# Performance work log

Measured on AMD Instinct MI355X. Metric: run time of the kernel, lower is better.

Reference implementation:

```python
import jax, jax.numpy as jnp
import numpy as np

B, C, H = 65536, 512, 8
HD = C // H  # head dim = 64
SCALE = HD ** -0.5


def setup_inputs() -> dict:
    key = jax.random.key(0)
    k1, k2, k3, k4 = jax.random.split(key, 4)
    x = jax.random.normal(k1, (B, 2, C), dtype=jnp.float32)
    W_kv = jax.random.normal(k2, (C, 2 * C), dtype=jnp.float32) * (C ** -0.5)
    W_proj = jax.random.normal(k3, (C, C), dtype=jnp.float32) * (C ** -0.5)
    b_proj = jax.random.normal(k4, (C,), dtype=jnp.float32) * 0.01
    return {"x": x, "W_kv": W_kv, "W_proj": W_proj, "b_proj": b_proj}


def _kv(tok, W_kv):
    # tok: [B, N, C] -> k, v each [B, H, N, hd]
    b, n, c = tok.shape
    kv = (tok @ W_kv).reshape(b, n, 2, H, HD)          # [B,N,2,H,hd]
    kv = jnp.transpose(kv, (2, 0, 3, 1, 4))            # [2,B,H,N,hd]
    return kv[0], kv[1]


def reference(x, W_kv, W_proj, b_proj):
    x_img = x[:, :1, :]   # [B,1,C]
    x_pps = x[:, 1:, :]   # [B,N,C], N==1 (required by original reshape)
    b, n, c = x_pps.shape

    k_img, v_img = _kv(x_img, W_kv)   # [B,H,N,hd] each
    k_pps, v_pps = _kv(x_pps, W_kv)

    q = jnp.transpose(x_pps.reshape(b, n, H, HD), (0, 2, 1, 3))  # [B,H,N,hd]

    attn = jnp.einsum('bhqd,bhkd->bhqk', q, k_pps) * SCALE
    attn = jax.nn.softmax(attn, axis=-1)
    out = jnp.einsum('bhqk,bhkd->bhqd', attn, v_img)             # [B,H,N,hd]
    out = jnp.transpose(out, (0, 2, 1, 3)).reshape(b, n, c)       # [B,N,C]
    return out @ W_proj + b_proj
```

## Files before the change

kernel.cpp:

```cpp
#include <hip/hip_runtime.h>
#include <stdint.h>

typedef __attribute__((ext_vector_type(4))) float f32x4;
typedef __attribute__((ext_vector_type(8))) __bf16 bf16x8;
typedef __attribute__((ext_vector_type(4))) __bf16 bf16x4;

static __device__ __forceinline__ unsigned short f2bf(float f) {
  union { float f; uint32_t u; } v; v.f = f;
  return (unsigned short)((v.u + 0x7fffu + ((v.u >> 16) & 1u)) >> 16);
}

__global__ __launch_bounds__(256) void prep_wc(
    const float* __restrict__ W_kv, const float* __restrict__ W_proj,
    unsigned short* __restrict__ WcPack)
{
  const int t = threadIdx.x;
  const int k0 = blockIdx.x * 4;
  const int col = t & 127;
  const int n = col * 4;
  const int kj = __builtin_amdgcn_readfirstlane((t >> 7) * 2);
  const float* __restrict__ wv0 = W_kv + (size_t)(k0 + kj) * 1024 + 512;
  const float* __restrict__ wv1 = wv0 + 1024;

  float a0a[4] = {}, a0b[4] = {}, a1a[4] = {}, a1b[4] = {};
  #pragma unroll 4
  for (int c = 0; c < 256; ++c) {
    const float s0 = wv0[c],        s1 = wv1[c];
    const float t0 = wv0[c + 256],  t1 = wv1[c + 256];
    const f32x4 p = *reinterpret_cast<const f32x4*>(W_proj + (size_t)c * 512 + n);
    const f32x4 q = *reinterpret_cast<const f32x4*>(W_proj + (size_t)(c + 256) * 512 + n);
    #pragma unroll
    for (int i = 0; i < 4; ++i) {
      a0a[i] += s0 * p[i]; a1a[i] += s1 * p[i];
      a0b[i] += t0 * q[i]; a1b[i] += t1 * q[i];
    }
  }

  #pragma unroll
  for (int j = 0; j < 2; ++j) {
    const int k = k0 + kj + j;
    const int ks = k >> 6, kk = k & 63;
    #pragma unroll
    for (int i = 0; i < 4; ++i) {
      const float val = j ? (a1a[i] + a1b[i]) : (a0a[i] + a0b[i]);
      const int nn = n + i;
      const int ct = nn >> 7, cc = nn & 127;
      const uint32_t boff = (uint32_t)(((cc << 7) + (kk << 1)) ^ ((cc & 7) << 4));
      WcPack[(size_t)(((ct << 3) + ks) << 13) + (boff >> 1)] = f2bf(val);
    }
  }
}

__global__ __launch_bounds__(256, 2) void gemm_main(
    const float* __restrict__ x, const unsigned short* __restrict__ WcPack,
    const float* __restrict__ b_proj, float* __restrict__ out)
{
  __shared__ unsigned short Alds[2][128 * 64];
  __shared__ unsigned short Blds[2][128 * 64];

  const int tid = threadIdx.x;
  const int rawb = (int)blockIdx.x;
  const int bid = ((rawb & 7) << 8) + (rawb >> 3);
  const int m0 = (bid >> 2) << 7;
  const int ct = bid & 3;
  const int n0 = ct << 7;

  const int lane = tid & 63;
  const int wave = tid >> 6;
  const int wr = wave >> 1, wc = wave & 1;
  const int l15 = lane & 15, l4 = lane >> 4;

  f32x4 acc[4][4] = {};

  const int arow = tid >> 4;
  const int af4 = tid & 15;

  auto issueB = [&](int bufi, int kt) {
    const char* g = reinterpret_cast<const char*>(WcPack) + (((ct << 3) + kt) << 14);
    char* l = reinterpret_cast<char*>(&Blds[bufi][0]);
    #pragma unroll
    for (int i = 0; i < 4; ++i) {
      const int off = (i << 12) + (tid << 4);
      __builtin_amdgcn_global_load_lds(
          (__attribute__((address_space(1))) void*)(void*)(g + off),
          (__attribute__((address_space(3))) void*)(void*)(l + off),
          16, 0, 0);
    }
  };
  auto loadA = [&](int kt, f32x4* tmp) {
    const float* src = x + (size_t)m0 * 1024 + (kt << 6);
    #pragma unroll
    for (int p = 0; p < 8; ++p) {
      const int row = arow + (p << 4);
      tmp[p] = *reinterpret_cast<const f32x4*>(src + (size_t)row * 1024 + (af4 << 2));
    }
  };
  auto writeA = [&](int bufi, const f32x4* tmp) {
    char* base = reinterpret_cast<char*>(&Alds[bufi][0]);
    #pragma unroll
    for (int p = 0; p < 8; ++p) {
      const int row = arow + (p << 4);
      const uint32_t boff = (uint32_t)(((row << 7) + (af4 << 3)) ^ ((row & 7) << 4));
      bf16x4 h;
      h[0] = (__bf16)tmp[p][0]; h[1] = (__bf16)tmp[p][1];
      h[2] = (__bf16)tmp[p][2]; h[3] = (__bf16)tmp[p][3];
      *reinterpret_cast<bf16x4*>(base + boff) = h;
    }
  };
  auto compute = [&](int bufi) {
    const char* Ab = reinterpret_cast<const char*>(&Alds[bufi][0]);
    const char* Bb = reinterpret_cast<const char*>(&Blds[bufi][0]);
    #pragma unroll
    for (int ks = 0; ks < 2; ++ks) {
      bf16x8 afr[4], bfr[4];
      #pragma unroll
      for (int i = 0; i < 4; ++i) {
        const int ar = (wr << 6) + (i << 4) + l15;
        const uint32_t ao = (uint32_t)(((ar << 7) + (ks << 6) + (l4 << 4)) ^ ((ar & 7) << 4));
        afr[i] = *reinterpret_cast<const bf16x8*>(Ab + ao);
        const int bc = (wc << 6) + (i << 4) + l15;
        const uint32_t bo = (uint32_t)(((bc << 7) + (ks << 6) + (l4 << 4)) ^ ((bc & 7) << 4));
        bfr[i] = *reinterpret_cast<const bf16x8*>(Bb + bo);
      }
      #pragma unroll
      for (int mi = 0; mi < 4; ++mi)
        #pragma unroll
        for (int ni = 0; ni < 4; ++ni)
          acc[mi][ni] = __builtin_amdgcn_mfma_f32_16x16x32_bf16(
              afr[mi], bfr[ni], acc[mi][ni], 0, 0, 0);
    }
  };

  {
    f32x4 tmp[8];
    issueB(0, 0);
    loadA(0, tmp);
    writeA(0, tmp);
  }
  __syncthreads();

  int buf = 0;
  for (int kt = 0; kt < 8; ++kt) {
    f32x4 nxt[8];
    if (kt < 7) { issueB(buf ^ 1, kt + 1); loadA(kt + 1, nxt); }
    compute(buf);
    if (kt < 7) writeA(buf ^ 1, nxt);
    __syncthreads();
    buf ^= 1;
  }

  const int cbase = n0 + (wc << 6) + l15;
  float bias[4];
  #pragma unroll
  for (int ni = 0; ni < 4; ++ni) bias[ni] = b_proj[cbase + (ni << 4)];
  const int rbase = m0 + (wr << 6) + (l4 << 2);
  #pragma unroll
  for (int mi = 0; mi < 4; ++mi) {
    #pragma unroll
    for (int ni = 0; ni < 4; ++ni) {
      const int cg = cbase + (ni << 4);
      #pragma unroll
      for (int rg = 0; rg < 4; ++rg) {
        const int row = rbase + (mi << 4) + rg;
        out[(size_t)row * 512 + cg] = acc[mi][ni][rg] + bias[ni];
      }
    }
  }
}

extern "C" void kernel_launch(void* const* d_in, const int* in_sizes, int n_in,
                              void* d_out, int out_size, void* d_ws, size_t ws_size,
                              hipStream_t stream) {
  const float* x      = (const float*)d_in[0];
  const float* W_kv   = (const float*)d_in[1];
  const float* W_proj = (const float*)d_in[2];
  const float* b_proj = (const float*)d_in[3];
  float* out = (float*)d_out;
  unsigned short* WcPack = (unsigned short*)d_ws;

  prep_wc<<<128, 256, 0, stream>>>(W_kv, W_proj, WcPack);
  gemm_main<<<2048, 256, 0, stream>>>(x, WcPack, b_proj, out);
}
```

Before: 455.0 us.

## Triple-buffer B tile with manual waitcnt and barrier pipeline

```diff
diff --git a/kernel.cpp b/kernel.cpp
--- a/kernel.cpp
+++ b/kernel.cpp
@@ -55,8 +55,8 @@
     const float* __restrict__ x, const unsigned short* __restrict__ WcPack,
     const float* __restrict__ b_proj, float* __restrict__ out)
 {
-  __shared__ unsigned short Alds[2][128 * 64];
-  __shared__ unsigned short Blds[2][128 * 64];
+  __shared__ __align__(16) unsigned short Alds[2][128 * 64];
+  __shared__ __align__(16) unsigned short Blds[3][128 * 64];
 
   const int tid = threadIdx.x;
   const int rawb = (int)blockIdx.x;
@@ -107,9 +107,9 @@
       *reinterpret_cast<bf16x4*>(base + boff) = h;
     }
   };
-  auto compute = [&](int bufi) {
-    const char* Ab = reinterpret_cast<const char*>(&Alds[bufi][0]);
-    const char* Bb = reinterpret_cast<const char*>(&Blds[bufi][0]);
+  auto compute = [&](int abuf, int bbuf) {
+    const char* Ab = reinterpret_cast<const char*>(&Alds[abuf][0]);
+    const char* Bb = reinterpret_cast<const char*>(&Blds[bbuf][0]);
     #pragma unroll
     for (int ks = 0; ks < 2; ++ks) {
       bf16x8 afr[4], bfr[4];
@@ -135,19 +135,28 @@
     f32x4 tmp[8];
     issueB(0, 0);
     loadA(0, tmp);
+    issueB(1, 1);
+    asm volatile("s_waitcnt vmcnt(4)" ::: "memory");
     writeA(0, tmp);
+    asm volatile("s_waitcnt lgkmcnt(0)" ::: "memory");
+    __builtin_amdgcn_s_barrier();
+    asm volatile("" ::: "memory");
   }
-  __syncthreads();
 
-  int buf = 0;
-  for (int kt = 0; kt < 8; ++kt) {
+  #pragma unroll
+  for (int kt = 0; kt < 7; ++kt) {
     f32x4 nxt[8];
-    if (kt < 7) { issueB(buf ^ 1, kt + 1); loadA(kt + 1, nxt); }
-    compute(buf);
-    if (kt < 7) writeA(buf ^ 1, nxt);
-    __syncthreads();
-    buf ^= 1;
+    loadA(kt + 1, nxt);
+    if (kt < 6) issueB((kt + 2) % 3, kt + 2);
+    compute(kt & 1, kt % 3);
+    if (kt < 6) asm volatile("s_waitcnt vmcnt(4)" ::: "memory");
+    else        asm volatile("s_waitcnt vmcnt(0)" ::: "memory");
+    writeA((kt + 1) & 1, nxt);
+    asm volatile("s_waitcnt lgkmcnt(0)" ::: "memory");
+    __builtin_amdgcn_s_barrier();
+    asm volatile("" ::: "memory");
   }
+  compute(7 & 1, 7 % 3);
 
   const int cbase = n0 + (wc << 6) + l15;
   float bias[4];
```

Result: no change. 450.9 us (-0.9%).
